# Kernel tuning notes

Hardware: AMD Instinct MI355X
Metric: run time of the kernel (lower is better)

The kernel has to match this reference:

```python
import jax, jax.numpy as jnp
import numpy as np

N_NODES = 100000
NEG_SLOPE = 0.2

def _glorot(key, shape):
    lim = float(np.sqrt(6.0 / (shape[0] + shape[-1])))
    return jax.random.uniform(key, shape, jnp.float32, -lim, lim)

def setup_inputs() -> dict:
    key = jax.random.key(0)
    ks = jax.random.split(key, 12)
    x = jax.random.normal(ks[0], (N_NODES, 128), jnp.float32)
    edge_index = jax.random.randint(ks[1], (2, 3200000), 0, N_NODES).astype(jnp.int64)
    # layer 1: in=128, heads=2, out=8
    W1 = _glorot(ks[2], (128, 16)); a_src1 = _glorot(ks[3], (2, 8)); a_dst1 = _glorot(ks[4], (2, 8)); b1 = jnp.zeros((16,), jnp.float32)
    # layer 2: in=16, heads=2, out=4
    W2 = _glorot(ks[5], (16, 8)); a_src2 = _glorot(ks[6], (2, 4)); a_dst2 = _glorot(ks[7], (2, 4)); b2 = jnp.zeros((8,), jnp.float32)
    # layer 3: in=8, heads=1, out=4
    W3 = _glorot(ks[8], (8, 4)); a_src3 = _glorot(ks[9], (1, 4)); a_dst3 = _glorot(ks[10], (1, 4)); b3 = jnp.zeros((4,), jnp.float32)
    Wc = _glorot(ks[11], (4, 2)); bc = jnp.zeros((2,), jnp.float32)
    return {"x": x, "edge_index": edge_index,
            "W1": W1, "a_src1": a_src1, "a_dst1": a_dst1, "b1": b1,
            "W2": W2, "a_src2": a_src2, "a_dst2": a_dst2, "b2": b2,
            "W3": W3, "a_src3": a_src3, "a_dst3": a_dst3, "b3": b3,
            "Wc": Wc, "bc": bc}

def gat_layer(x, src, dst, W, a_src, a_dst, b, H, C):
    # PyG GATConv: linear -> per-node attention terms -> per-edge leaky_relu -> segment softmax over dst -> scatter-sum
    N = x.shape[0]
    h = (x @ W).reshape(N, H, C)                         # [N,H,C]
    alpha_s = jnp.sum(h * a_src, axis=-1)                # [N,H]
    alpha_d = jnp.sum(h * a_dst, axis=-1)                # [N,H]
    e = jax.nn.leaky_relu(alpha_s[src] + alpha_d[dst], NEG_SLOPE)  # [E,H]
    m = jax.ops.segment_max(e, dst, num_segments=N)      # [N,H]
    ex = jnp.exp(e - m[dst])
    denom = jax.ops.segment_sum(ex, dst, num_segments=N)
    alpha = ex / (denom[dst] + 1e-16)                    # [E,H]
    out = jax.ops.segment_sum(h[src] * alpha[:, :, None], dst, num_segments=N)  # [N,H,C]
    return out.reshape(N, H * C) + b

def reference(x, edge_index, W1, a_src1, a_dst1, b1, W2, a_src2, a_dst2, b2, W3, a_src3, a_dst3, b3, Wc, bc):
    N = x.shape[0]
    loop = jnp.arange(N, dtype=edge_index.dtype)
    src = jnp.concatenate([edge_index[0], loop])  # add_self_loops=True (PyG default)
    dst = jnp.concatenate([edge_index[1], loop])
    h = jax.nn.relu(gat_layer(x, src, dst, W1, a_src1, a_dst1, b1, 2, 8))
    h = jax.nn.relu(gat_layer(h, src, dst, W2, a_src2, a_dst2, b2, 2, 4))
    # dropout p=0.5 is identity in eval mode
    h = gat_layer(h, src, dst, W3, a_src3, a_dst3, b3, 1, 4)
    return h @ Wc + bc
```

## Files before the change

kernel.cpp:

```cpp
#include <hip/hip_runtime.h>

#define TB 256
#define NGRP 8
#define NB_P 512
#define TBP 256
#define NBKT 256
#define SORT_T 1024
#define STG_CAP 14336
#define STG2_CAP 6400

typedef int      i4v __attribute__((ext_vector_type(4)));
typedef float    f4v __attribute__((ext_vector_type(4)));
typedef _Float16 h4v __attribute__((ext_vector_type(4)));
typedef _Float16 h8v __attribute__((ext_vector_type(8)));

struct __align__(16) Rec2 { _Float16 h[8]; float as[2]; float pad[2]; };
struct __align__(16) Rec3 { _Float16 h[4]; float as; float pad; };

static __device__ __forceinline__ float leaky(float x) {
  return x > 0.f ? x : 0.2f * x;
}


__global__ void __launch_bounds__(TB)
k_bcount_node1(const int* __restrict__ dstA, int* __restrict__ cnt,
               int E4, int E, unsigned M, int CH4,
               const float* __restrict__ xin, const float* __restrict__ W1,
               const float* __restrict__ a_src, const float* __restrict__ a_dst,
               _Float16* __restrict__ hout, float* __restrict__ as_,
               float* __restrict__ ad_, int N) {
  __shared__ __align__(16) char smem[8448];
  if (blockIdx.x < NB_P) {
    int* lc = (int*)smem;
    for (int i = threadIdx.x; i < 4 * NBKT; i += TBP) lc[i] = 0;
    __syncthreads();
    int* lcw = lc + (threadIdx.x >> 6) * NBKT;
    const int bstart = blockIdx.x * CH4;
    const int bend = min(E4, bstart + CH4);
    const i4v* d4 = reinterpret_cast<const i4v*>(dstA);
    for (int i = bstart + threadIdx.x; i < bend; i += TBP) {
      i4v d = __builtin_nontemporal_load(&d4[i]);
#pragma unroll
      for (int k = 0; k < 4; ++k) atomicAdd(&lcw[__umulhi((unsigned)d[k], M)], 1);
    }
    if (blockIdx.x == NB_P - 1) {
      for (int t = E4 * 4 + threadIdx.x; t < E; t += TBP)
        atomicAdd(&lcw[__umulhi((unsigned)dstA[t], M)], 1);
    }
    __syncthreads();
    for (int b = threadIdx.x; b < NBKT; b += TBP)
      cnt[b * NB_P + blockIdx.x] = lc[b] + lc[NBKT + b] + lc[2 * NBKT + b] + lc[3 * NBKT + b];
  } else {
    constexpr int IN = 128, OUT = 16, SPLIT = 4, NPB = TB / SPLIT, PIN4 = IN / SPLIT / 4;
    float* Ws = (float*)smem;
    float* As = (float*)(smem + 8192);
    float* Ad = (float*)(smem + 8256);
    const int bid = blockIdx.x - NB_P;
    for (int i = threadIdx.x; i < IN * OUT; i += TB) Ws[i] = W1[i];
    if (threadIdx.x < OUT) {
      As[threadIdx.x] = a_src[threadIdx.x];
      Ad[threadIdx.x] = a_dst[threadIdx.x];
    }
    __syncthreads();
    const int j = threadIdx.x & (SPLIT - 1);
    const int n = bid * NPB + threadIdx.x / SPLIT;
    if (n >= N) return;
    float acc[OUT];
#pragma unroll
    for (int q = 0; q < OUT; ++q) acc[q] = 0.f;
    const f4v* x4 = reinterpret_cast<const f4v*>(xin + (size_t)n * IN + j * (IN / SPLIT));
#pragma unroll
    for (int k4 = 0; k4 < PIN4; ++k4) {
      f4v xv = __builtin_nontemporal_load(&x4[k4]);
      const int kb = j * (IN / SPLIT) + 4 * k4;
#pragma unroll
      for (int q = 0; q < OUT; ++q) {
        acc[q] += xv[0] * Ws[(kb + 0) * OUT + q];
        acc[q] += xv[1] * Ws[(kb + 1) * OUT + q];
        acc[q] += xv[2] * Ws[(kb + 2) * OUT + q];
        acc[q] += xv[3] * Ws[(kb + 3) * OUT + q];
      }
    }
#pragma unroll
    for (int o = 1; o < SPLIT; o <<= 1) {
#pragma unroll
      for (int q = 0; q < OUT; ++q) acc[q] += __shfl_xor(acc[q], o);
    }
    if (j < OUT / 4) {
      h4v v;
      v[0] = (_Float16)acc[4 * j + 0];
      v[1] = (_Float16)acc[4 * j + 1];
      v[2] = (_Float16)acc[4 * j + 2];
      v[3] = (_Float16)acc[4 * j + 3];
      reinterpret_cast<h4v*>(hout + (size_t)n * OUT)[j] = v;
    }
    if (j < 2) {
      float ss = 0.f, dd = 0.f;
#pragma unroll
      for (int c = 0; c < 8; ++c) {
        ss += acc[j * 8 + c] * As[j * 8 + c];
        dd += acc[j * 8 + c] * Ad[j * 8 + c];
      }
      as_[n * 2 + j] = ss;
      ad_[n * 2 + j] = dd;
    }
  }
}

__global__ void k_bscan1(const int* __restrict__ cnt, int* __restrict__ off,
                         int* __restrict__ colTotal) {
  __shared__ int sh[NB_P];
  const int t = threadIdx.x;
  const int b = blockIdx.x;
  int v = cnt[b * NB_P + t];
  sh[t] = v;
  __syncthreads();
  for (int o = 1; o < NB_P; o <<= 1) {
    int u = (t >= o) ? sh[t - o] : 0;
    __syncthreads();
    sh[t] += u;
    __syncthreads();
  }
  off[b * NB_P + t] = sh[t] - v;
  if (t == NB_P - 1) colTotal[b] = sh[t];
}

__global__ void k_bscan2(const int* __restrict__ colTotal, int* __restrict__ bucketBase) {
  __shared__ int sh[NBKT];
  const int t = threadIdx.x;
  int v = colTotal[t];
  sh[t] = v;
  __syncthreads();
  for (int o = 1; o < NBKT; o <<= 1) {
    int u = (t >= o) ? sh[t - o] : 0;
    __syncthreads();
    sh[t] += u;
    __syncthreads();
  }
  bucketBase[t] = sh[t] - v;
  if (t == NBKT - 1) bucketBase[NBKT] = sh[t];
}

__global__ void k_bscatter(const int* __restrict__ srcA, const int* __restrict__ dstA,
                           const int* __restrict__ cnt, const int* __restrict__ off,
                           const int* __restrict__ bucketBase, int* __restrict__ epk,
                           int E4, int E, unsigned M, int R, int CH4) {
  __shared__ int loff[NBKT + 1];
  __shared__ int lcur[NBKT];
  __shared__ int gbase[NBKT];
  __shared__ int stg[STG2_CAP];
  const int t = threadIdx.x;
  {
    int v = cnt[t * NB_P + blockIdx.x];
    loff[t] = v;
    __syncthreads();
    for (int o = 1; o < NBKT; o <<= 1) {
      int u = (t >= o) ? loff[t - o] : 0;
      __syncthreads();
      loff[t] += u;
      __syncthreads();
    }
    int incl = loff[t];
    __syncthreads();
    loff[t] = incl - v;
    lcur[t] = incl - v;
    if (t == NBKT - 1) loff[NBKT] = incl;
    gbase[t] = bucketBase[t] + off[t * NB_P + blockIdx.x];
  }
  __syncthreads();
  const int bstart = blockIdx.x * CH4;
  const int bend = min(E4, bstart + CH4);
  const i4v* d4 = reinterpret_cast<const i4v*>(dstA);
  const i4v* s4 = reinterpret_cast<const i4v*>(srcA);
  for (int i = bstart + t; i < bend; i += TBP) {
    i4v d = __builtin_nontemporal_load(&d4[i]);
    i4v sv = __builtin_nontemporal_load(&s4[i]);
#pragma unroll
    for (int k = 0; k < 4; ++k) {
      int dd = d[k];
      int b = __umulhi((unsigned)dd, M);
      int pos = atomicAdd(&lcur[b], 1);
      stg[pos] = ((dd - b * R) << 17) | sv[k];
    }
  }
  if (blockIdx.x == NB_P - 1) {
    for (int i = E4 * 4 + t; i < E; i += TBP) {
      int dd = dstA[i];
      int b = __umulhi((unsigned)dd, M);
      int pos = atomicAdd(&lcur[b], 1);
      stg[pos] = ((dd - b * R) << 17) | srcA[i];
    }
  }
  __syncthreads();
  const int total = loff[NBKT];
  for (int i = t; i < total; i += TBP) {
    int loQ = 0, hiQ = NBKT;
#pragma unroll
    for (int it = 0; it < 8; ++it) {
      int mid = (loQ + hiQ) >> 1;
      if (loff[mid] <= i) loQ = mid; else hiQ = mid;
    }
    epk[gbase[loQ] + (i - loff[loQ])] = stg[i];
  }
}

__global__ void k_bsort(const int* __restrict__ epk, const int* __restrict__ bucketBase,
                        int* __restrict__ rowStart, int* __restrict__ colIdx,
                        int N, int R, int E) {
  __shared__ int sc[512];
  __shared__ int stg[STG_CAP];
  const int b = (blockIdx.x & (NGRP - 1)) * (NBKT / NGRP) + (blockIdx.x >> 3);
  const int lo = bucketBase[b], hi = bucketBase[b + 1];
  const int cnt = hi - lo;
  const int nodeLo = b * R;
  const int nN = min(R, N - nodeLo);
  const int t = threadIdx.x;
  if (t < 512) sc[t] = 0;
  __syncthreads();
  for (int i = lo + t; i < hi; i += SORT_T) {
    int pk = __builtin_nontemporal_load(&epk[i]);
    atomicAdd(&sc[pk >> 17], 1);
  }
  __syncthreads();
  int own = (t < 512) ? sc[t] : 0;
  for (int o = 1; o < 512; o <<= 1) {
    int u = (t < 512 && t >= o) ? sc[t - o] : 0;
    __syncthreads();
    if (t < 512) sc[t] += u;
    __syncthreads();
  }
  if (t < nN) rowStart[nodeLo + t] = lo + sc[t] - own;
  if (b == NBKT - 1 && t == 0) rowStart[N] = E;
  if (t < 512) sc[t] -= own;
  __syncthreads();
  if (cnt <= STG_CAP) {
    for (int i = lo + t; i < hi; i += SORT_T) {
      int pk = epk[i];
      int pos = atomicAdd(&sc[pk >> 17], 1);
      stg[pos] = pk & 0x1FFFF;
    }
    __syncthreads();
    for (int i = t; i < cnt; i += SORT_T) colIdx[lo + i] = stg[i];
  } else {
    for (int i = lo + t; i < hi; i += SORT_T) {
      int pk = epk[i];
      int pos = lo + atomicAdd(&sc[pk >> 17], 1);
      colIdx[pos] = pk & 0x1FFFF;
    }
  }
}


__global__ void k_edge12(const int* __restrict__ rowStart, const int* __restrict__ colIdx,
                         const _Float16* __restrict__ h1, const float* __restrict__ as_,
                         const float* __restrict__ ad_, const float* __restrict__ b1,
                         const float* __restrict__ W2, const float* __restrict__ as2w,
                         const float* __restrict__ ad2w, Rec2* __restrict__ r2,
                         float* __restrict__ ad2, int N, int R8) {
  constexpr int L = 2, S = 4, LS = 8, NPB = TB / LS;
  __shared__ float Ws2[128], A2s[8], A2d[8], B1s[16];
  if (threadIdx.x < 128) Ws2[threadIdx.x] = W2[threadIdx.x];
  if (threadIdx.x < 8) {
    A2s[threadIdx.x] = as2w[threadIdx.x];
    A2d[threadIdx.x] = ad2w[threadIdx.x];
  }
  if (threadIdx.x < 16) B1s[threadIdx.x] = b1[threadIdx.x];
  __syncthreads();
  const int g = blockIdx.x & (NGRP - 1);
  const int lb = blockIdx.x / NGRP;
  const int lane = threadIdx.x % LS;
  const int sub = lane >> 1;
  const int j = lane & 1;
  const int n = g * R8 + lb * NPB + threadIdx.x / LS;
  const int nEnd = min((g + 1) * R8, N);
  if (n >= nEnd) return;
  const float adv = ad_[n * 2 + j];
  const int start = rowStart[n];
  const int end = rowStart[n + 1];
  float s = 0.f, acc[8];
#pragma unroll
  for (int q = 0; q < 8; ++q) acc[q] = 0.f;
  if (sub == 0) {
    float p = __expf(leaky(as_[n * 2 + j] + adv));
    h8v a0 = reinterpret_cast<const h8v*>(h1 + (size_t)n * 16)[j];
    s = p;
#pragma unroll
    for (int q = 0; q < 8; ++q) acc[q] = p * (float)a0[q];
  }
  const int base = start & ~3;
  const int nch = (end - base + 3) >> 2;
  i4v cv;
  if (sub < nch) cv = *reinterpret_cast<const i4v*>(colIdx + base + 4 * sub);
  for (int t = sub; t < nch; t += S) {
    i4v nxt = cv;
    if (t + S < nch) nxt = *reinterpret_cast<const i4v*>(colIdx + base + 4 * (t + S));
    const int i0 = base + 4 * t;
#pragma unroll
    for (int k = 0; k < 4; ++k) {
      const bool ok = (i0 + k >= start) && (i0 + k < end);
      const int src = ok ? cv[k] : n;
      h8v hv = reinterpret_cast<const h8v*>(h1 + (size_t)src * 16)[j];
      float e = as_[src * 2 + j];
      float p = ok ? __expf(leaky(e + adv)) : 0.f;
      s += p;
#pragma unroll
      for (int q = 0; q < 8; ++q) acc[q] += p * (float)hv[q];
    }
    cv = nxt;
  }
#pragma unroll
  for (int off = L; off < LS; off <<= 1) {
    s += __shfl_xor(s, off);
#pragma unroll
    for (int q = 0; q < 8; ++q) acc[q] += __shfl_xor(acc[q], off);
  }
  if (sub == 0) {
    float inv = 1.f / (s + 1e-16f);
    float o1v[8];
#pragma unroll
    for (int q = 0; q < 8; ++q) o1v[q] = fmaxf(acc[q] * inv + B1s[j * 8 + q], 0.f);
    float h2p[8];
#pragma unroll
    for (int q = 0; q < 8; ++q) {
      float tacc = 0.f;
#pragma unroll
      for (int c = 0; c < 8; ++c) tacc += o1v[c] * Ws2[(j * 8 + c) * 8 + q];
      h2p[q] = tacc;
    }
    float h2f[8];
#pragma unroll
    for (int q = 0; q < 8; ++q) h2f[q] = h2p[q] + __shfl_xor(h2p[q], 1);
    h4v v;
#pragma unroll
    for (int q = 0; q < 4; ++q) v[q] = (_Float16)h2f[j * 4 + q];
    reinterpret_cast<h4v*>(r2[n].h)[j] = v;
    float ss = 0.f, dd = 0.f;
#pragma unroll
    for (int c = 0; c < 4; ++c) {
      ss += h2f[j * 4 + c] * A2s[j * 4 + c];
      dd += h2f[j * 4 + c] * A2d[j * 4 + c];
    }
    r2[n].as[j] = ss;
    ad2[n * 2 + j] = dd;
  }
}


__global__ void k_edge23(const int* __restrict__ rowStart, const int* __restrict__ colIdx,
                         const Rec2* __restrict__ r2, const float* __restrict__ ad_,
                         const float* __restrict__ b2, const float* __restrict__ W3,
                         const float* __restrict__ as3w, const float* __restrict__ ad3w,
                         Rec3* __restrict__ r3, float* __restrict__ ad3, int N, int R8) {
  constexpr int L = 2, S = 4, LS = 8, NPB = TB / LS;
  __shared__ float Ws3[32], A3s[4], A3d[4], B2s[8];
  if (threadIdx.x < 32) Ws3[threadIdx.x] = W3[threadIdx.x];
  if (threadIdx.x < 4) {
    A3s[threadIdx.x] = as3w[threadIdx.x];
    A3d[threadIdx.x] = ad3w[threadIdx.x];
  }
  if (threadIdx.x < 8) B2s[threadIdx.x] = b2[threadIdx.x];
  __syncthreads();
  const int g = blockIdx.x & (NGRP - 1);
  const int lb = blockIdx.x / NGRP;
  const int lane = threadIdx.x % LS;
  const int sub = lane >> 1;
  const int j = lane & 1;
  const int n = g * R8 + lb * NPB + threadIdx.x / LS;
  const int nEnd = min((g + 1) * R8, N);
  if (n >= nEnd) return;
  const float adv = ad_[n * 2 + j];
  const int start = rowStart[n];
  const int end = rowStart[n + 1];
  float s = 0.f, acc[4];
#pragma unroll
  for (int q = 0; q < 4; ++q) acc[q] = 0.f;
  if (sub == 0) {
    float p = __expf(leaky(r2[n].as[j] + adv));
    h4v a0 = reinterpret_cast<const h4v*>(r2[n].h)[j];
    s = p;
#pragma unroll
    for (int q = 0; q < 4; ++q) acc[q] = p * (float)a0[q];
  }
  const int base = start & ~3;
  const int nch = (end - base + 3) >> 2;
  i4v cv;
  if (sub < nch) cv = *reinterpret_cast<const i4v*>(colIdx + base + 4 * sub);
  for (int t = sub; t < nch; t += S) {
    i4v nxt = cv;
    if (t + S < nch) nxt = *reinterpret_cast<const i4v*>(colIdx + base + 4 * (t + S));
    const int i0 = base + 4 * t;
#pragma unroll
    for (int k = 0; k < 4; ++k) {
      const bool ok = (i0 + k >= start) && (i0 + k < end);
      const int src = ok ? cv[k] : n;
      h4v hv = reinterpret_cast<const h4v*>(r2[src].h)[j];
      float e = r2[src].as[j];
      float p = ok ? __expf(leaky(e + adv)) : 0.f;
      s += p;
#pragma unroll
      for (int q = 0; q < 4; ++q) acc[q] += p * (float)hv[q];
    }
    cv = nxt;
  }
#pragma unroll
  for (int off = L; off < LS; off <<= 1) {
    s += __shfl_xor(s, off);
#pragma unroll
    for (int q = 0; q < 4; ++q) acc[q] += __shfl_xor(acc[q], off);
  }
  if (sub == 0) {
    float inv = 1.f / (s + 1e-16f);
    float o2v[4];
#pragma unroll
    for (int q = 0; q < 4; ++q) o2v[q] = fmaxf(acc[q] * inv + B2s[j * 4 + q], 0.f);
    float h3p[4];
#pragma unroll
    for (int q = 0; q < 4; ++q) {
      float tacc = 0.f;
#pragma unroll
      for (int c = 0; c < 4; ++c) tacc += o2v[c] * Ws3[(j * 4 + c) * 4 + q];
      h3p[q] = tacc;
    }
    float h3f[4];
#pragma unroll
    for (int q = 0; q < 4; ++q) h3f[q] = h3p[q] + __shfl_xor(h3p[q], 1);
    if (j == 0) {
      Rec3 rec;
#pragma unroll
      for (int q = 0; q < 4; ++q) rec.h[q] = (_Float16)h3f[q];
      float ss = 0.f, dd = 0.f;
#pragma unroll
      for (int c = 0; c < 4; ++c) {
        ss += h3f[c] * A3s[c];
        dd += h3f[c] * A3d[c];
      }
      rec.as = ss;
      rec.pad = 0.f;
      r3[n] = rec;
      ad3[n] = dd;
    }
  }
}


__global__ void k_edge3(const int* __restrict__ rowStart, const int* __restrict__ colIdx,
                        const Rec3* __restrict__ r3, const float* __restrict__ ad_,
                        const float* __restrict__ b3, const float* __restrict__ Wc,
                        const float* __restrict__ bc, float* __restrict__ out,
                        int N, int R8) {
  constexpr int S = 8;
  constexpr int NPB = TB / S;
  const int g = blockIdx.x & (NGRP - 1);
  const int lb = blockIdx.x / NGRP;
  const int sub = threadIdx.x % S;
  const int n = g * R8 + lb * NPB + threadIdx.x / S;
  const int nEnd = min((g + 1) * R8, N);
  if (n >= nEnd) return;
  const float adv = ad_[n];
  const int start = rowStart[n];
  const int end = rowStart[n + 1];
  float s = 0.f, acc0 = 0.f, acc1 = 0.f, acc2 = 0.f, acc3 = 0.f;
  if (sub == 0) {
    Rec3 rec = r3[n];
    float p = __expf(leaky(rec.as + adv));
    s = p;
    acc0 = p * (float)rec.h[0];
    acc1 = p * (float)rec.h[1];
    acc2 = p * (float)rec.h[2];
    acc3 = p * (float)rec.h[3];
  }
  const int base = start & ~3;
  const int nch = (end - base + 3) >> 2;
  i4v cv;
  if (sub < nch) cv = *reinterpret_cast<const i4v*>(colIdx + base + 4 * sub);
  for (int t = sub; t < nch; t += S) {
    i4v nxt = cv;
    if (t + S < nch) nxt = *reinterpret_cast<const i4v*>(colIdx + base + 4 * (t + S));
    const int i0 = base + 4 * t;
#pragma unroll
    for (int k = 0; k < 4; ++k) {
      const bool ok = (i0 + k >= start) && (i0 + k < end);
      const int src = ok ? cv[k] : n;
      Rec3 rec = r3[src];
      float p = ok ? __expf(leaky(rec.as + adv)) : 0.f;
      s += p;
      acc0 += p * (float)rec.h[0];
      acc1 += p * (float)rec.h[1];
      acc2 += p * (float)rec.h[2];
      acc3 += p * (float)rec.h[3];
    }
    cv = nxt;
  }
#pragma unroll
  for (int off = 1; off < S; off <<= 1) {
    s += __shfl_xor(s, off);
    acc0 += __shfl_xor(acc0, off);
    acc1 += __shfl_xor(acc1, off);
    acc2 += __shfl_xor(acc2, off);
    acc3 += __shfl_xor(acc3, off);
  }
  if (sub == 0) {
    float inv = 1.f / (s + 1e-16f);
    float o0 = acc0 * inv + b3[0];
    float o1 = acc1 * inv + b3[1];
    float o2 = acc2 * inv + b3[2];
    float o3 = acc3 * inv + b3[3];
    float2 r;
    r.x = o0 * Wc[0] + o1 * Wc[2] + o2 * Wc[4] + o3 * Wc[6] + bc[0];
    r.y = o0 * Wc[1] + o1 * Wc[3] + o2 * Wc[5] + o3 * Wc[7] + bc[1];
    reinterpret_cast<float2*>(out)[n] = r;
  }
}


extern "C" void kernel_launch(void* const* d_in, const int* in_sizes, int n_in,
                              void* d_out, int out_size, void* d_ws, size_t ws_size,
                              hipStream_t stream) {
  const float* x    = (const float*)d_in[0];
  const int*   ei   = (const int*)d_in[1];
  const float* W1   = (const float*)d_in[2];
  const float* as1w = (const float*)d_in[3];
  const float* ad1w = (const float*)d_in[4];
  const float* b1   = (const float*)d_in[5];
  const float* W2   = (const float*)d_in[6];
  const float* as2w = (const float*)d_in[7];
  const float* ad2w = (const float*)d_in[8];
  const float* b2   = (const float*)d_in[9];
  const float* W3   = (const float*)d_in[10];
  const float* as3w = (const float*)d_in[11];
  const float* ad3w = (const float*)d_in[12];
  const float* b3   = (const float*)d_in[13];
  const float* Wc   = (const float*)d_in[14];
  const float* bc   = (const float*)d_in[15];
  float* out = (float*)d_out;

  const int N = in_sizes[0] / 128;
  const int E = in_sizes[1] / 2;
  const int* srcA = ei;
  const int* dstA = ei + E;

  char* p = (char*)d_ws;
  auto alloc = [&](size_t bytes) -> void* {
    void* r = (void*)p;
    p += (bytes + 255) & ~(size_t)255;
    return r;
  };
  int* cnt        = (int*)alloc((size_t)NBKT * NB_P * 4);
  int* off        = (int*)alloc((size_t)NBKT * NB_P * 4);
  int* colTotal   = (int*)alloc(NBKT * 4);
  int* bucketBase = (int*)alloc((NBKT + 1) * 4);
  int* rowStart   = (int*)alloc((size_t)(N + 1) * 4);
  int* epk        = (int*)alloc((size_t)E * 4);
  int* colIdx     = (int*)alloc((size_t)E * 4 + 256);
  _Float16* h1 = (_Float16*)alloc((size_t)N * 16 * 2);
  float* as1 = (float*)alloc((size_t)N * 2 * 4);
  float* ad1 = (float*)alloc((size_t)N * 2 * 4);
  Rec2* r2   = (Rec2*)alloc((size_t)N * sizeof(Rec2));
  float* ad2 = (float*)alloc((size_t)N * 2 * 4);
  Rec3* r3   = (Rec3*)alloc((size_t)N * sizeof(Rec3));
  float* ad3 = (float*)alloc((size_t)N * 4);

  const int R   = (N + NBKT - 1) / NBKT;
  const unsigned M = (unsigned)(((1ULL << 32) + R - 1) / R);
  const int R8  = R * (NBKT / NGRP);
  const int E4  = E >> 2;
  const int CH4 = (E4 + NB_P - 1) / NB_P;

  const int nb1 = (N + (TB / 4) - 1) / (TB / 4);
  const int ge8 = NGRP * ((R8 + (TB / 8) - 1) / (TB / 8));

  k_bcount_node1<<<NB_P + nb1, TB, 0, stream>>>(dstA, cnt, E4, E, M, CH4,
                                                x, W1, as1w, ad1w, h1, as1, ad1, N);
  k_bscan1<<<NBKT, NB_P, 0, stream>>>(cnt, off, colTotal);
  k_bscan2<<<1, NBKT, 0, stream>>>(colTotal, bucketBase);
  k_bscatter<<<NB_P, TBP, 0, stream>>>(srcA, dstA, cnt, off, bucketBase, epk, E4, E, M, R, CH4);
  k_bsort<<<NBKT, SORT_T, 0, stream>>>(epk, bucketBase, rowStart, colIdx, N, R, E);

  k_edge12<<<ge8, TB, 0, stream>>>(rowStart, colIdx, h1, as1, ad1, b1, W2, as2w, ad2w,
                                   r2, ad2, N, R8);
  k_edge23<<<ge8, TB, 0, stream>>>(rowStart, colIdx, r2, ad2, b2, W3, as3w, ad3w,
                                   r3, ad3, N, R8);
  k_edge3<<<ge8, TB, 0, stream>>>(rowStart, colIdx, r3, ad3, b3, Wc, bc, out, N, R8);
}
```

Measured before the change: 172.2 us.

## Fuse bucket count and local scatter into one pass, gather per-bucket in sort

The bucket-count kernel now also does each block's local bucket scatter into shared memory and writes the block-local sorted chunk to a private buffer. The separate global scatter kernel is removed. The sort kernel gathers its bucket's edges from each block's chunk, using a binary search over the per-block offsets. This drops one kernel launch and one full pass over the edge arrays, at the cost of a larger shared-memory footprint in the fused kernel, which may lower occupancy. The sort also loses its fallback path for buckets that overflow the staging buffer, and each element fetch now pays a 9-step search.

New measurement: 168.8 us. No clear change (-2.0%).

```diff
diff --git a/kernel.cpp b/kernel.cpp
--- a/kernel.cpp
+++ b/kernel.cpp
@@ -7,7 +7,7 @@
 #define NBKT 256
 #define SORT_T 1024
 #define STG_CAP 14336
-#define STG2_CAP 6400
+#define STG2_CAP 6656
 
 typedef int      i4v __attribute__((ext_vector_type(4)));
 typedef float    f4v __attribute__((ext_vector_type(4)));
@@ -23,47 +23,97 @@
 
 
 __global__ void __launch_bounds__(TB)
-k_bcount_node1(const int* __restrict__ dstA, int* __restrict__ cnt,
-               int E4, int E, unsigned M, int CH4,
-               const float* __restrict__ xin, const float* __restrict__ W1,
-               const float* __restrict__ a_src, const float* __restrict__ a_dst,
-               _Float16* __restrict__ hout, float* __restrict__ as_,
-               float* __restrict__ ad_, int N) {
-  __shared__ __align__(16) char smem[8448];
+k_scatter_node1(const int* __restrict__ srcA, const int* __restrict__ dstA,
+                int* __restrict__ cnt, int* __restrict__ loffG,
+                int* __restrict__ epkPriv, int E4, int E, unsigned M, int R,
+                int CH4, int CHP,
+                const float* __restrict__ xin, const float* __restrict__ W1,
+                const float* __restrict__ a_src, const float* __restrict__ a_dst,
+                _Float16* __restrict__ hout, float* __restrict__ as_,
+                float* __restrict__ ad_, int N) {
+  __shared__ __align__(16) char smem[33552];
+  const int t = threadIdx.x;
   if (blockIdx.x < NB_P) {
-    int* lc = (int*)smem;
-    for (int i = threadIdx.x; i < 4 * NBKT; i += TBP) lc[i] = 0;
-    __syncthreads();
-    int* lcw = lc + (threadIdx.x >> 6) * NBKT;
-    const int bstart = blockIdx.x * CH4;
+    const int kblk = blockIdx.x;
+    int* lc   = (int*)smem;
+    int* loff = (int*)(smem + 4096);
+    int* lcur = (int*)(smem + 5136);
+    int* stg  = (int*)(smem + 6160);
+    for (int i = t; i < 4 * NBKT; i += TBP) lc[i] = 0;
+    __syncthreads();
+    int* lcw = lc + (t >> 6) * NBKT;
+    const int bstart = kblk * CH4;
     const int bend = min(E4, bstart + CH4);
     const i4v* d4 = reinterpret_cast<const i4v*>(dstA);
-    for (int i = bstart + threadIdx.x; i < bend; i += TBP) {
-      i4v d = __builtin_nontemporal_load(&d4[i]);
+    const i4v* s4 = reinterpret_cast<const i4v*>(srcA);
+    for (int i = bstart + t; i < bend; i += TBP) {
+      i4v d = d4[i];
 #pragma unroll
       for (int k = 0; k < 4; ++k) atomicAdd(&lcw[__umulhi((unsigned)d[k], M)], 1);
     }
-    if (blockIdx.x == NB_P - 1) {
-      for (int t = E4 * 4 + threadIdx.x; t < E; t += TBP)
-        atomicAdd(&lcw[__umulhi((unsigned)dstA[t], M)], 1);
-    }
-    __syncthreads();
-    for (int b = threadIdx.x; b < NBKT; b += TBP)
-      cnt[b * NB_P + blockIdx.x] = lc[b] + lc[NBKT + b] + lc[2 * NBKT + b] + lc[3 * NBKT + b];
+    if (kblk == NB_P - 1) {
+      for (int i = E4 * 4 + t; i < E; i += TBP)
+        atomicAdd(&lcw[__umulhi((unsigned)dstA[i], M)], 1);
+    }
+    __syncthreads();
+    int c = 0;
+    if (t < NBKT) {
+      c = lc[t] + lc[NBKT + t] + lc[2 * NBKT + t] + lc[3 * NBKT + t];
+      loff[t] = c;
+    }
+    __syncthreads();
+    for (int o = 1; o < NBKT; o <<= 1) {
+      int u = (t < NBKT && t >= o) ? loff[t - o] : 0;
+      __syncthreads();
+      if (t < NBKT) loff[t] += u;
+      __syncthreads();
+    }
+    if (t < NBKT) {
+      int excl = loff[t] - c;
+      cnt[t * NB_P + kblk] = c;
+      loffG[kblk * NBKT + t] = excl;
+      lcur[t] = excl;
+      loff[t] = excl;
+      if (t == NBKT - 1) loff[NBKT] = excl + c;
+    }
+    __syncthreads();
+    for (int i = bstart + t; i < bend; i += TBP) {
+      i4v d = d4[i];
+      i4v sv = __builtin_nontemporal_load(&s4[i]);
+#pragma unroll
+      for (int k = 0; k < 4; ++k) {
+        int dd = d[k];
+        int b = __umulhi((unsigned)dd, M);
+        int pos = atomicAdd(&lcur[b], 1);
+        stg[pos] = ((dd - b * R) << 17) | sv[k];
+      }
+    }
+    if (kblk == NB_P - 1) {
+      for (int i = E4 * 4 + t; i < E; i += TBP) {
+        int dd = dstA[i];
+        int b = __umulhi((unsigned)dd, M);
+        int pos = atomicAdd(&lcur[b], 1);
+        stg[pos] = ((dd - b * R) << 17) | srcA[i];
+      }
+    }
+    __syncthreads();
+    const int total = loff[NBKT];
+    int* dst = epkPriv + (size_t)kblk * CHP;
+    for (int i = t; i < total; i += TBP) dst[i] = stg[i];
   } else {
     constexpr int IN = 128, OUT = 16, SPLIT = 4, NPB = TB / SPLIT, PIN4 = IN / SPLIT / 4;
     float* Ws = (float*)smem;
     float* As = (float*)(smem + 8192);
     float* Ad = (float*)(smem + 8256);
     const int bid = blockIdx.x - NB_P;
-    for (int i = threadIdx.x; i < IN * OUT; i += TB) Ws[i] = W1[i];
-    if (threadIdx.x < OUT) {
-      As[threadIdx.x] = a_src[threadIdx.x];
-      Ad[threadIdx.x] = a_dst[threadIdx.x];
-    }
-    __syncthreads();
-    const int j = threadIdx.x & (SPLIT - 1);
-    const int n = bid * NPB + threadIdx.x / SPLIT;
+    for (int i = t; i < IN * OUT; i += TB) Ws[i] = W1[i];
+    if (t < OUT) {
+      As[t] = a_src[t];
+      Ad[t] = a_dst[t];
+    }
+    __syncthreads();
+    const int j = t & (SPLIT - 1);
+    const int n = bid * NPB + t / SPLIT;
     if (n >= N) return;
     float acc[OUT];
 #pragma unroll
@@ -141,84 +191,37 @@
   if (t == NBKT - 1) bucketBase[NBKT] = sh[t];
 }
 
-__global__ void k_bscatter(const int* __restrict__ srcA, const int* __restrict__ dstA,
-                           const int* __restrict__ cnt, const int* __restrict__ off,
-                           const int* __restrict__ bucketBase, int* __restrict__ epk,
-                           int E4, int E, unsigned M, int R, int CH4) {
-  __shared__ int loff[NBKT + 1];
-  __shared__ int lcur[NBKT];
-  __shared__ int gbase[NBKT];
-  __shared__ int stg[STG2_CAP];
-  const int t = threadIdx.x;
-  {
-    int v = cnt[t * NB_P + blockIdx.x];
-    loff[t] = v;
-    __syncthreads();
-    for (int o = 1; o < NBKT; o <<= 1) {
-      int u = (t >= o) ? loff[t - o] : 0;
-      __syncthreads();
-      loff[t] += u;
-      __syncthreads();
-    }
-    int incl = loff[t];
-    __syncthreads();
-    loff[t] = incl - v;
-    lcur[t] = incl - v;
-    if (t == NBKT - 1) loff[NBKT] = incl;
-    gbase[t] = bucketBase[t] + off[t * NB_P + blockIdx.x];
-  }
-  __syncthreads();
-  const int bstart = blockIdx.x * CH4;
-  const int bend = min(E4, bstart + CH4);
-  const i4v* d4 = reinterpret_cast<const i4v*>(dstA);
-  const i4v* s4 = reinterpret_cast<const i4v*>(srcA);
-  for (int i = bstart + t; i < bend; i += TBP) {
-    i4v d = __builtin_nontemporal_load(&d4[i]);
-    i4v sv = __builtin_nontemporal_load(&s4[i]);
-#pragma unroll
-    for (int k = 0; k < 4; ++k) {
-      int dd = d[k];
-      int b = __umulhi((unsigned)dd, M);
-      int pos = atomicAdd(&lcur[b], 1);
-      stg[pos] = ((dd - b * R) << 17) | sv[k];
-    }
-  }
-  if (blockIdx.x == NB_P - 1) {
-    for (int i = E4 * 4 + t; i < E; i += TBP) {
-      int dd = dstA[i];
-      int b = __umulhi((unsigned)dd, M);
-      int pos = atomicAdd(&lcur[b], 1);
-      stg[pos] = ((dd - b * R) << 17) | srcA[i];
-    }
-  }
-  __syncthreads();
-  const int total = loff[NBKT];
-  for (int i = t; i < total; i += TBP) {
-    int loQ = 0, hiQ = NBKT;
-#pragma unroll
-    for (int it = 0; it < 8; ++it) {
-      int mid = (loQ + hiQ) >> 1;
-      if (loff[mid] <= i) loQ = mid; else hiQ = mid;
-    }
-    epk[gbase[loQ] + (i - loff[loQ])] = stg[i];
-  }
-}
-
-__global__ void k_bsort(const int* __restrict__ epk, const int* __restrict__ bucketBase,
+__global__ void k_bsort(const int* __restrict__ epkPriv, const int* __restrict__ off,
+                        const int* __restrict__ loffG, const int* __restrict__ bucketBase,
                         int* __restrict__ rowStart, int* __restrict__ colIdx,
-                        int N, int R, int E) {
+                        int N, int R, int E, int CHP) {
+  __shared__ int offRow[NB_P];
+  __shared__ int loffCol[NB_P];
   __shared__ int sc[512];
   __shared__ int stg[STG_CAP];
   const int b = (blockIdx.x & (NGRP - 1)) * (NBKT / NGRP) + (blockIdx.x >> 3);
   const int lo = bucketBase[b], hi = bucketBase[b + 1];
-  const int cnt = hi - lo;
+  const int cntB = hi - lo;
   const int nodeLo = b * R;
   const int nN = min(R, N - nodeLo);
   const int t = threadIdx.x;
+  if (t < NB_P) {
+    offRow[t] = off[b * NB_P + t];
+    loffCol[t] = loffG[t * NBKT + b];
+  }
   if (t < 512) sc[t] = 0;
   __syncthreads();
-  for (int i = lo + t; i < hi; i += SORT_T) {
-    int pk = __builtin_nontemporal_load(&epk[i]);
+  auto fetch = [&](int i) -> int {
+    int loQ = 0, hiQ = NB_P;
+#pragma unroll
+    for (int it = 0; it < 9; ++it) {
+      int mid = (loQ + hiQ) >> 1;
+      if (offRow[mid] <= i) loQ = mid; else hiQ = mid;
+    }
+    return epkPriv[(size_t)loQ * CHP + loffCol[loQ] + (i - offRow[loQ])];
+  };
+  for (int i = t; i < cntB; i += SORT_T) {
+    int pk = fetch(i);
     atomicAdd(&sc[pk >> 17], 1);
   }
   __syncthreads();
@@ -233,21 +236,13 @@
   if (b == NBKT - 1 && t == 0) rowStart[N] = E;
   if (t < 512) sc[t] -= own;
   __syncthreads();
-  if (cnt <= STG_CAP) {
-    for (int i = lo + t; i < hi; i += SORT_T) {
-      int pk = epk[i];
-      int pos = atomicAdd(&sc[pk >> 17], 1);
-      stg[pos] = pk & 0x1FFFF;
-    }
-    __syncthreads();
-    for (int i = t; i < cnt; i += SORT_T) colIdx[lo + i] = stg[i];
-  } else {
-    for (int i = lo + t; i < hi; i += SORT_T) {
-      int pk = epk[i];
-      int pos = lo + atomicAdd(&sc[pk >> 17], 1);
-      colIdx[pos] = pk & 0x1FFFF;
-    }
-  }
+  for (int i = t; i < cntB; i += SORT_T) {
+    int pk = fetch(i);
+    int pos = atomicAdd(&sc[pk >> 17], 1);
+    stg[pos] = pk & 0x1FFFF;
+  }
+  __syncthreads();
+  for (int i = t; i < cntB; i += SORT_T) colIdx[lo + i] = stg[i];
 }
 
 
@@ -545,12 +540,17 @@
     p += (bytes + 255) & ~(size_t)255;
     return r;
   };
+  const int E4  = E >> 2;
+  const int CH4 = (E4 + NB_P - 1) / NB_P;
+  const int CHP = CH4 * 4 + 8;
+
   int* cnt        = (int*)alloc((size_t)NBKT * NB_P * 4);
   int* off        = (int*)alloc((size_t)NBKT * NB_P * 4);
+  int* loffG      = (int*)alloc((size_t)NB_P * NBKT * 4);
   int* colTotal   = (int*)alloc(NBKT * 4);
   int* bucketBase = (int*)alloc((NBKT + 1) * 4);
   int* rowStart   = (int*)alloc((size_t)(N + 1) * 4);
-  int* epk        = (int*)alloc((size_t)E * 4);
+  int* epkPriv    = (int*)alloc((size_t)NB_P * CHP * 4);
   int* colIdx     = (int*)alloc((size_t)E * 4 + 256);
   _Float16* h1 = (_Float16*)alloc((size_t)N * 16 * 2);
   float* as1 = (float*)alloc((size_t)N * 2 * 4);
@@ -563,18 +563,17 @@
   const int R   = (N + NBKT - 1) / NBKT;
   const unsigned M = (unsigned)(((1ULL << 32) + R - 1) / R);
   const int R8  = R * (NBKT / NGRP);
-  const int E4  = E >> 2;
-  const int CH4 = (E4 + NB_P - 1) / NB_P;
 
   const int nb1 = (N + (TB / 4) - 1) / (TB / 4);
   const int ge8 = NGRP * ((R8 + (TB / 8) - 1) / (TB / 8));
 
-  k_bcount_node1<<<NB_P + nb1, TB, 0, stream>>>(dstA, cnt, E4, E, M, CH4,
-                                                x, W1, as1w, ad1w, h1, as1, ad1, N);
+  k_scatter_node1<<<NB_P + nb1, TB, 0, stream>>>(srcA, dstA, cnt, loffG, epkPriv,
+                                                 E4, E, M, R, CH4, CHP,
+                                                 x, W1, as1w, ad1w, h1, as1, ad1, N);
   k_bscan1<<<NBKT, NB_P, 0, stream>>>(cnt, off, colTotal);
   k_bscan2<<<1, NBKT, 0, stream>>>(colTotal, bucketBase);
-  k_bscatter<<<NB_P, TBP, 0, stream>>>(srcA, dstA, cnt, off, bucketBase, epk, E4, E, M, R, CH4);
-  k_bsort<<<NBKT, SORT_T, 0, stream>>>(epk, bucketBase, rowStart, colIdx, N, R, E);
+  k_bsort<<<NBKT, SORT_T, 0, stream>>>(epkPriv, off, loffG, bucketBase, rowStart,
+                                       colIdx, N, R, E, CHP);
 
   k_edge12<<<ge8, TB, 0, stream>>>(rowStart, colIdx, h1, as1, ad1, b1, W2, as2w, ad2w,
                                    r2, ad2, N, R8);
```
